# Kernel tuning notes

Measured on AMD Instinct MI355X. Metric: run time of the kernel, lower is better.

## Reference

```python
import jax, jax.numpy as jnp
import numpy as np

B, L, H = 512, 1000, 128


def _lstm_cell(x_t, h, c, w_ih, w_hh, b_ih, b_hh):
    # PyTorch LSTMCell: gates = x @ W_ih^T + b_ih + h @ W_hh^T + b_hh, gate order i,f,g,o
    gates = x_t @ w_ih.T + b_ih + h @ w_hh.T + b_hh  # [B, 4H]
    i, f, g, o = jnp.split(gates, 4, axis=-1)
    i = jax.nn.sigmoid(i)
    f = jax.nn.sigmoid(f)
    g = jnp.tanh(g)
    o = jax.nn.sigmoid(o)
    c_new = f * c + i * g
    h_new = o * jnp.tanh(c_new)
    return h_new, c_new


def setup_inputs() -> dict:
    key = jax.random.key(0)
    ks = jax.random.split(key, 12)
    s = 1.0 / np.sqrt(H)  # torch default uniform(-1/sqrt(H), 1/sqrt(H))
    u = lambda k, shp: jax.random.uniform(k, shp, jnp.float32, -s, s)
    return {
        "x": jax.random.normal(ks[0], (B, L), jnp.float32),
        "w_ih1": u(ks[1], (4 * H, 1)),
        "w_hh1": u(ks[2], (4 * H, H)),
        "b_ih1": u(ks[3], (4 * H,)),
        "b_hh1": u(ks[4], (4 * H,)),
        "w_ih2": u(ks[5], (4 * H, H)),
        "w_hh2": u(ks[6], (4 * H, H)),
        "b_ih2": u(ks[7], (4 * H,)),
        "b_hh2": u(ks[8], (4 * H,)),
        "w_lin": u(ks[9], (1, H)),
        "b_lin": u(ks[10], (1,)),
    }


def reference(x, w_ih1, w_hh1, b_ih1, b_hh1, w_ih2, w_hh2, b_ih2, b_hh2, w_lin, b_lin):
    n = x.shape[0]
    h = w_hh1.shape[1]
    zeros = jnp.zeros((n, h), x.dtype)
    init = (zeros, zeros, zeros, zeros)  # h1, c1, h2, c2

    def step(carry, x_t):
        h1, c1, h2, c2 = carry
        h1, c1 = _lstm_cell(x_t, h1, c1, w_ih1, w_hh1, b_ih1, b_hh1)
        h2, c2 = _lstm_cell(h1, h2, c2, w_ih2, w_hh2, b_ih2, b_hh2)
        out = h2 @ w_lin.T + b_lin  # [B, 1]
        return (h1, c1, h2, c2), out[:, 0]

    xs = x.T[:, :, None]  # [L, B, 1]
    _, outs = jax.lax.scan(step, init, xs)  # outs: [L, B]
    return outs.T  # [B, L]
```

## Files before the change

### kernel.cpp

```cpp
#include <hip/hip_runtime.h>

#define B_ 512
#define L_ 1000
#define H_ 128
#define G_ 512

typedef _Float16 v8h __attribute__((ext_vector_type(8)));
typedef _Float16 h2t __attribute__((ext_vector_type(2)));
typedef float v4f __attribute__((ext_vector_type(4)));

__device__ __forceinline__ float sigmoid_f(float x) {
  return __builtin_amdgcn_rcpf(1.0f + __builtin_amdgcn_exp2f(-1.4426950408889634f * x));
}
__device__ __forceinline__ float tanh_f(float x) {
  return 1.0f - 2.0f * __builtin_amdgcn_rcpf(1.0f + __builtin_amdgcn_exp2f(2.8853900817779268f * x));
}

#define FB_KT 144

#define MFMA16(a, b, c) __builtin_amdgcn_mfma_f32_16x16x32_f16((a), (b), (c), 0, 0, 0)

__global__ __launch_bounds__(512, 2) void lstm_mfma(
    const float* __restrict__ x,
    const float* __restrict__ w_ih1,
    const float* __restrict__ w_hh1,
    const float* __restrict__ b_ih1,
    const float* __restrict__ b_hh1,
    const float* __restrict__ w_ih2,
    const float* __restrict__ w_hh2,
    const float* __restrict__ b_ih2,
    const float* __restrict__ b_hh2,
    const float* __restrict__ w_lin,
    const float* __restrict__ b_lin,
    float* __restrict__ out)
{
  __shared__ __align__(16) float xlds[2][L_];
  __shared__ __align__(16) float olds[2 * L_];
  __shared__ __align__(16) float gbuf1[2][G_];
  __shared__ __align__(16) float gbuf2[2][G_];
  __shared__ __align__(16) unsigned char hb1[4 * FB_KT];
  __shared__ __align__(16) unsigned char hb2[4 * FB_KT];
  __shared__ __align__(16) float wxb[G_];
  __shared__ __align__(16) float bbb1[G_];
  __shared__ __align__(16) float bbb2[G_];
  __shared__ __align__(16) float wlb[H_];

  const int tid  = threadIdx.x;
  const int wv   = tid >> 6;
  const int lane = tid & 63;
  const int quad = lane >> 4;
  const int m15  = lane & 15;
  const int r0   = blockIdx.x * 2;
  const int e    = 2 * lane;

  for (int i = tid; i < 2 * L_; i += 512) ((float*)xlds)[i] = x[r0 * L_ + i];
  ((float*)gbuf1)[tid]       = 0.f;
  ((float*)gbuf1)[tid + 512] = 0.f;
  wxb[tid]  = w_ih1[tid];
  bbb1[tid] = b_ih1[tid] + b_hh1[tid];
  bbb2[tid] = b_ih2[tid] + b_hh2[tid];
  if (tid < H_) wlb[tid] = w_lin[tid];
  if (tid < 144) {
    ((unsigned*)hb1)[tid] = 0u;
    ((unsigned*)hb2)[tid] = 0u;
  }
  const float blv = b_lin[0];

  v8h A1f[4][4], A2if[4][4], A2hf[4][4];
#pragma unroll
  for (int mt = 0; mt < 4; ++mt) {
    const int grow = ((4 * wv + mt) * 16 + m15) * H_;
#pragma unroll
    for (int kt = 0; kt < 4; ++kt) {
      const int koff = kt * 32 + quad * 8;
      float4 a, b;
      a = *(const float4*)(w_hh1 + grow + koff);
      b = *(const float4*)(w_hh1 + grow + koff + 4);
      A1f[mt][kt] = v8h{(_Float16)a.x, (_Float16)a.y, (_Float16)a.z, (_Float16)a.w,
                        (_Float16)b.x, (_Float16)b.y, (_Float16)b.z, (_Float16)b.w};
      a = *(const float4*)(w_ih2 + grow + koff);
      b = *(const float4*)(w_ih2 + grow + koff + 4);
      A2if[mt][kt] = v8h{(_Float16)a.x, (_Float16)a.y, (_Float16)a.z, (_Float16)a.w,
                         (_Float16)b.x, (_Float16)b.y, (_Float16)b.z, (_Float16)b.w};
      a = *(const float4*)(w_hh2 + grow + koff);
      b = *(const float4*)(w_hh2 + grow + koff + 4);
      A2hf[mt][kt] = v8h{(_Float16)a.x, (_Float16)a.y, (_Float16)a.z, (_Float16)a.w,
                         (_Float16)b.x, (_Float16)b.y, (_Float16)b.z, (_Float16)b.w};
    }
  }

  float c1x = 0.f, c1y = 0.f;
  float c2x = 0.f, c2y = 0.f;

  const int hwo = (lane >> 4) * FB_KT + ((lane >> 2) & 3) * 32 + (lane & 3) * 4;
  const int roff = quad * 32 + (m15 & 1) * 16;

  __syncthreads();

  for (int t = 0; t <= L_; ++t) {
    if (tid < 128) {
      if (t < L_) {
        const int row = tid >> 6;
        const float xv = xlds[row][t];
        const float* g1 = gbuf1[row];
        float2 gi = *(const float2*)&g1[e];
        float2 gf = *(const float2*)&g1[128 + e];
        float2 gg = *(const float2*)&g1[256 + e];
        float2 go = *(const float2*)&g1[384 + e];
        float2 wxi = *(const float2*)&wxb[e],       bi = *(const float2*)&bbb1[e];
        float2 wxf = *(const float2*)&wxb[128 + e], bf = *(const float2*)&bbb1[128 + e];
        float2 wxg = *(const float2*)&wxb[256 + e], bg = *(const float2*)&bbb1[256 + e];
        float2 wxo = *(const float2*)&wxb[384 + e], bo = *(const float2*)&bbb1[384 + e];
        float i0 = sigmoid_f(gi.x + wxi.x * xv + bi.x);
        float i1 = sigmoid_f(gi.y + wxi.y * xv + bi.y);
        float f0 = sigmoid_f(gf.x + wxf.x * xv + bf.x);
        float f1 = sigmoid_f(gf.y + wxf.y * xv + bf.y);
        float g0 = tanh_f(gg.x + wxg.x * xv + bg.x);
        float g1v = tanh_f(gg.y + wxg.y * xv + bg.y);
        float o0 = sigmoid_f(go.x + wxo.x * xv + bo.x);
        float o1 = sigmoid_f(go.y + wxo.y * xv + bo.y);
        c1x = f0 * c1x + i0 * g0;
        c1y = f1 * c1y + i1 * g1v;
        h2t hp = h2t{(_Float16)(o0 * tanh_f(c1x)), (_Float16)(o1 * tanh_f(c1y))};
        *(unsigned*)(hb1 + row * 16 + hwo) = __builtin_bit_cast(unsigned, hp);
      }
    } else if (tid < 256) {
      if (t > 0) {
        const int row = (tid >> 6) & 1;
        const float* g2 = gbuf2[row];
        float2 gi = *(const float2*)&g2[e];
        float2 gf = *(const float2*)&g2[128 + e];
        float2 gg = *(const float2*)&g2[256 + e];
        float2 go = *(const float2*)&g2[384 + e];
        float2 bi = *(const float2*)&bbb2[e];
        float2 bf = *(const float2*)&bbb2[128 + e];
        float2 bg = *(const float2*)&bbb2[256 + e];
        float2 bo = *(const float2*)&bbb2[384 + e];
        float i0 = sigmoid_f(gi.x + bi.x);
        float i1 = sigmoid_f(gi.y + bi.y);
        float f0 = sigmoid_f(gf.x + bf.x);
        float f1 = sigmoid_f(gf.y + bf.y);
        float g0 = tanh_f(gg.x + bg.x);
        float g1v = tanh_f(gg.y + bg.y);
        float o0 = sigmoid_f(go.x + bo.x);
        float o1 = sigmoid_f(go.y + bo.y);
        c2x = f0 * c2x + i0 * g0;
        c2y = f1 * c2y + i1 * g1v;
        float h0 = o0 * tanh_f(c2x);
        float h1 = o1 * tanh_f(c2y);
        h2t hp = h2t{(_Float16)h0, (_Float16)h1};
        *(unsigned*)(hb2 + row * 16 + hwo) = __builtin_bit_cast(unsigned, hp);
        float2 wlv = *(const float2*)&wlb[e];
        float p2 = h0 * wlv.x + h1 * wlv.y;
#pragma unroll
        for (int s = 1; s < 64; s <<= 1) p2 += __shfl_xor(p2, s, 64);
        if (lane == 0) olds[row * L_ + (t - 1)] = p2 + blv;
      }
    }
    __syncthreads();

    if (t < L_) {
      v4f a2[4], a1[4];
#pragma unroll
      for (int m = 0; m < 4; ++m) { a2[m] = v4f{0, 0, 0, 0}; a1[m] = v4f{0, 0, 0, 0}; }
      __builtin_amdgcn_s_setprio(1);
#pragma unroll
      for (int kt = 0; kt < 4; ++kt) {
        v8h b1 = *(const v8h*)(hb1 + kt * FB_KT + roff);
        v8h b2 = *(const v8h*)(hb2 + kt * FB_KT + roff);
#pragma unroll
        for (int m = 0; m < 4; ++m) {
          a2[m] = MFMA16(A2if[m][kt], b1, a2[m]);
          a2[m] = MFMA16(A2hf[m][kt], b2, a2[m]);
          a1[m] = MFMA16(A1f[m][kt],  b1, a1[m]);
        }
      }
      __builtin_amdgcn_s_setprio(0);
      if (m15 < 2) {
#pragma unroll
        for (int m = 0; m < 4; ++m) {
          *(v4f*)&gbuf2[m15][(4 * wv + m) * 16 + quad * 4] = a2[m];
          *(v4f*)&gbuf1[m15][(4 * wv + m) * 16 + quad * 4] = a1[m];
        }
      }
    }
    __syncthreads();
  }

  for (int i = tid; i < 2 * L_; i += 512) out[r0 * L_ + i] = olds[i];
}

extern "C" void kernel_launch(void* const* d_in, const int* in_sizes, int n_in,
                              void* d_out, int out_size, void* d_ws, size_t ws_size,
                              hipStream_t stream) {
  const float* x     = (const float*)d_in[0];
  const float* w_ih1 = (const float*)d_in[1];
  const float* w_hh1 = (const float*)d_in[2];
  const float* b_ih1 = (const float*)d_in[3];
  const float* b_hh1 = (const float*)d_in[4];
  const float* w_ih2 = (const float*)d_in[5];
  const float* w_hh2 = (const float*)d_in[6];
  const float* b_ih2 = (const float*)d_in[7];
  const float* b_hh2 = (const float*)d_in[8];
  const float* w_lin = (const float*)d_in[9];
  const float* b_lin = (const float*)d_in[10];

  lstm_mfma<<<B_ / 2, 512, 0, stream>>>(
      x, w_ih1, w_hh1, b_ih1, b_hh1, w_ih2, w_hh2, b_ih2, b_hh2,
      w_lin, b_lin, (float*)d_out);
}
```

Measured before the change: 1.604 ms.

## Overlap LSTM layer elementwise phases with the other layer's MFMA

Splits each timestep's single MFMA phase into two halves. The layer-1 elementwise update now runs alongside the layer-2 gate MFMAs, and the layer-2 elementwise update runs alongside the layer-1 recurrent MFMAs. The h1 fp16 buffer is double-buffered so the layer-2 MFMA can read the previous step's h1 while layer 1 writes the new one. The goal is to stop MFMA-idle waves from waiting behind the serial activation math between barriers. The cost is more complex buffer indexing, and the layer-2 MFMA does one wasted pass at t=0.

Result: slower. 1.733 ms (+8.0%).

```diff
diff --git a/kernel.cpp b/kernel.cpp
--- a/kernel.cpp
+++ b/kernel.cpp
@@ -38,7 +38,7 @@
   __shared__ __align__(16) float olds[2 * L_];
   __shared__ __align__(16) float gbuf1[2][G_];
   __shared__ __align__(16) float gbuf2[2][G_];
-  __shared__ __align__(16) unsigned char hb1[4 * FB_KT];
+  __shared__ __align__(16) unsigned char hb1[2][4 * FB_KT];
   __shared__ __align__(16) unsigned char hb2[4 * FB_KT];
   __shared__ __align__(16) float wxb[G_];
   __shared__ __align__(16) float bbb1[G_];
@@ -60,10 +60,8 @@
   bbb1[tid] = b_ih1[tid] + b_hh1[tid];
   bbb2[tid] = b_ih2[tid] + b_hh2[tid];
   if (tid < H_) wlb[tid] = w_lin[tid];
-  if (tid < 144) {
-    ((unsigned*)hb1)[tid] = 0u;
-    ((unsigned*)hb2)[tid] = 0u;
-  }
+  if (tid < 288) ((unsigned*)hb1)[tid] = 0u;
+  if (tid < 144) ((unsigned*)hb2)[tid] = 0u;
   const float blv = b_lin[0];
 
   v8h A1f[4][4], A2if[4][4], A2hf[4][4];
@@ -98,90 +96,104 @@
   __syncthreads();
 
   for (int t = 0; t <= L_; ++t) {
-    if (tid < 128) {
-      if (t < L_) {
-        const int row = tid >> 6;
-        const float xv = xlds[row][t];
-        const float* g1 = gbuf1[row];
-        float2 gi = *(const float2*)&g1[e];
-        float2 gf = *(const float2*)&g1[128 + e];
-        float2 gg = *(const float2*)&g1[256 + e];
-        float2 go = *(const float2*)&g1[384 + e];
-        float2 wxi = *(const float2*)&wxb[e],       bi = *(const float2*)&bbb1[e];
-        float2 wxf = *(const float2*)&wxb[128 + e], bf = *(const float2*)&bbb1[128 + e];
-        float2 wxg = *(const float2*)&wxb[256 + e], bg = *(const float2*)&bbb1[256 + e];
-        float2 wxo = *(const float2*)&wxb[384 + e], bo = *(const float2*)&bbb1[384 + e];
-        float i0 = sigmoid_f(gi.x + wxi.x * xv + bi.x);
-        float i1 = sigmoid_f(gi.y + wxi.y * xv + bi.y);
-        float f0 = sigmoid_f(gf.x + wxf.x * xv + bf.x);
-        float f1 = sigmoid_f(gf.y + wxf.y * xv + bf.y);
-        float g0 = tanh_f(gg.x + wxg.x * xv + bg.x);
-        float g1v = tanh_f(gg.y + wxg.y * xv + bg.y);
-        float o0 = sigmoid_f(go.x + wxo.x * xv + bo.x);
-        float o1 = sigmoid_f(go.y + wxo.y * xv + bo.y);
-        c1x = f0 * c1x + i0 * g0;
-        c1y = f1 * c1y + i1 * g1v;
-        h2t hp = h2t{(_Float16)(o0 * tanh_f(c1x)), (_Float16)(o1 * tanh_f(c1y))};
-        *(unsigned*)(hb1 + row * 16 + hwo) = __builtin_bit_cast(unsigned, hp);
-      }
-    } else if (tid < 256) {
-      if (t > 0) {
-        const int row = (tid >> 6) & 1;
-        const float* g2 = gbuf2[row];
-        float2 gi = *(const float2*)&g2[e];
-        float2 gf = *(const float2*)&g2[128 + e];
-        float2 gg = *(const float2*)&g2[256 + e];
-        float2 go = *(const float2*)&g2[384 + e];
-        float2 bi = *(const float2*)&bbb2[e];
-        float2 bf = *(const float2*)&bbb2[128 + e];
-        float2 bg = *(const float2*)&bbb2[256 + e];
-        float2 bo = *(const float2*)&bbb2[384 + e];
-        float i0 = sigmoid_f(gi.x + bi.x);
-        float i1 = sigmoid_f(gi.y + bi.y);
-        float f0 = sigmoid_f(gf.x + bf.x);
-        float f1 = sigmoid_f(gf.y + bf.y);
-        float g0 = tanh_f(gg.x + bg.x);
-        float g1v = tanh_f(gg.y + bg.y);
-        float o0 = sigmoid_f(go.x + bo.x);
-        float o1 = sigmoid_f(go.y + bo.y);
-        c2x = f0 * c2x + i0 * g0;
-        c2y = f1 * c2y + i1 * g1v;
-        float h0 = o0 * tanh_f(c2x);
-        float h1 = o1 * tanh_f(c2y);
-        h2t hp = h2t{(_Float16)h0, (_Float16)h1};
-        *(unsigned*)(hb2 + row * 16 + hwo) = __builtin_bit_cast(unsigned, hp);
-        float2 wlv = *(const float2*)&wlb[e];
-        float p2 = h0 * wlv.x + h1 * wlv.y;
-#pragma unroll
-        for (int s = 1; s < 64; s <<= 1) p2 += __shfl_xor(p2, s, 64);
-        if (lane == 0) olds[row * L_ + (t - 1)] = p2 + blv;
-      }
-    }
-    __syncthreads();
-
-    if (t < L_) {
-      v4f a2[4], a1[4];
-#pragma unroll
-      for (int m = 0; m < 4; ++m) { a2[m] = v4f{0, 0, 0, 0}; a1[m] = v4f{0, 0, 0, 0}; }
+    if (tid < 128 && t < L_) {
+      const int row = tid >> 6;
+      const float xv = xlds[row][t];
+      const float* g1 = gbuf1[row];
+      float2 gi = *(const float2*)&g1[e];
+      float2 gf = *(const float2*)&g1[128 + e];
+      float2 gg = *(const float2*)&g1[256 + e];
+      float2 go = *(const float2*)&g1[384 + e];
+      float2 wxi = *(const float2*)&wxb[e],       bi = *(const float2*)&bbb1[e];
+      float2 wxf = *(const float2*)&wxb[128 + e], bf = *(const float2*)&bbb1[128 + e];
+      float2 wxg = *(const float2*)&wxb[256 + e], bg = *(const float2*)&bbb1[256 + e];
+      float2 wxo = *(const float2*)&wxb[384 + e], bo = *(const float2*)&bbb1[384 + e];
+      float i0 = sigmoid_f(gi.x + wxi.x * xv + bi.x);
+      float i1 = sigmoid_f(gi.y + wxi.y * xv + bi.y);
+      float f0 = sigmoid_f(gf.x + wxf.x * xv + bf.x);
+      float f1 = sigmoid_f(gf.y + wxf.y * xv + bf.y);
+      float g0 = tanh_f(gg.x + wxg.x * xv + bg.x);
+      float g1v = tanh_f(gg.y + wxg.y * xv + bg.y);
+      float o0 = sigmoid_f(go.x + wxo.x * xv + bo.x);
+      float o1 = sigmoid_f(go.y + wxo.y * xv + bo.y);
+      c1x = f0 * c1x + i0 * g0;
+      c1y = f1 * c1y + i1 * g1v;
+      h2t hp = h2t{(_Float16)(o0 * tanh_f(c1x)), (_Float16)(o1 * tanh_f(c1y))};
+      *(unsigned*)(&hb1[t & 1][0] + row * 16 + hwo) = __builtin_bit_cast(unsigned, hp);
+    }
+    {
+      v4f a2[4];
+#pragma unroll
+      for (int m = 0; m < 4; ++m) a2[m] = v4f{0, 0, 0, 0};
+      const unsigned char* b1p = &hb1[(t + 1) & 1][0];
       __builtin_amdgcn_s_setprio(1);
 #pragma unroll
       for (int kt = 0; kt < 4; ++kt) {
-        v8h b1 = *(const v8h*)(hb1 + kt * FB_KT + roff);
         v8h b2 = *(const v8h*)(hb2 + kt * FB_KT + roff);
+        v8h b1 = *(const v8h*)(b1p + kt * FB_KT + roff);
 #pragma unroll
         for (int m = 0; m < 4; ++m) {
+          a2[m] = MFMA16(A2hf[m][kt], b2, a2[m]);
           a2[m] = MFMA16(A2if[m][kt], b1, a2[m]);
-          a2[m] = MFMA16(A2hf[m][kt], b2, a2[m]);
-          a1[m] = MFMA16(A1f[m][kt],  b1, a1[m]);
         }
       }
       __builtin_amdgcn_s_setprio(0);
       if (m15 < 2) {
 #pragma unroll
-        for (int m = 0; m < 4; ++m) {
+        for (int m = 0; m < 4; ++m)
           *(v4f*)&gbuf2[m15][(4 * wv + m) * 16 + quad * 4] = a2[m];
+      }
+    }
+    __syncthreads();
+
+    if (tid >= 128 && tid < 256 && t > 0) {
+      const int row = (tid >> 6) & 1;
+      const float* g2 = gbuf2[row];
+      float2 gi = *(const float2*)&g2[e];
+      float2 gf = *(const float2*)&g2[128 + e];
+      float2 gg = *(const float2*)&g2[256 + e];
+      float2 go = *(const float2*)&g2[384 + e];
+      float2 bi = *(const float2*)&bbb2[e];
+      float2 bf = *(const float2*)&bbb2[128 + e];
+      float2 bg = *(const float2*)&bbb2[256 + e];
+      float2 bo = *(const float2*)&bbb2[384 + e];
+      float i0 = sigmoid_f(gi.x + bi.x);
+      float i1 = sigmoid_f(gi.y + bi.y);
+      float f0 = sigmoid_f(gf.x + bf.x);
+      float f1 = sigmoid_f(gf.y + bf.y);
+      float g0 = tanh_f(gg.x + bg.x);
+      float g1v = tanh_f(gg.y + bg.y);
+      float o0 = sigmoid_f(go.x + bo.x);
+      float o1 = sigmoid_f(go.y + bo.y);
+      c2x = f0 * c2x + i0 * g0;
+      c2y = f1 * c2y + i1 * g1v;
+      float h0 = o0 * tanh_f(c2x);
+      float h1 = o1 * tanh_f(c2y);
+      h2t hp = h2t{(_Float16)h0, (_Float16)h1};
+      *(unsigned*)(hb2 + row * 16 + hwo) = __builtin_bit_cast(unsigned, hp);
+      float2 wlv = *(const float2*)&wlb[e];
+      float p2 = h0 * wlv.x + h1 * wlv.y;
+#pragma unroll
+      for (int s = 1; s < 64; s <<= 1) p2 += __shfl_xor(p2, s, 64);
+      if (lane == 0) olds[row * L_ + (t - 1)] = p2 + blv;
+    }
+    if (t < L_) {
+      v4f a1[4];
+#pragma unroll
+      for (int m = 0; m < 4; ++m) a1[m] = v4f{0, 0, 0, 0};
+      const unsigned char* b1p = &hb1[t & 1][0];
+      __builtin_amdgcn_s_setprio(1);
+#pragma unroll
+      for (int kt = 0; kt < 4; ++kt) {
+        v8h b1 = *(const v8h*)(b1p + kt * FB_KT + roff);
+#pragma unroll
+        for (int m = 0; m < 4; ++m) a1[m] = MFMA16(A1f[m][kt], b1, a1[m]);
+      }
+      __builtin_amdgcn_s_setprio(0);
+      if (m15 < 2) {
+#pragma unroll
+        for (int m = 0; m < 4; ++m)
           *(v4f*)&gbuf1[m15][(4 * wv + m) * 16 + quad * 4] = a1[m];
-        }
       }
     }
     __syncthreads();
```

## Fuse LSTM gate activations into MFMA accumulators with gate-interleaved row mapping

Applied to the files above, without the earlier changes.

Weight rows are remapped so each wave's four MFMA tiles hold the i, f, g, o gates for the same 16 hidden units. Each lane can then apply the cell update directly from its accumulator registers, which removes the gbuf round trip through LDS and the separate activation threads. Biases are folded in as the accumulator's initial value, and h buffers are double-buffered in LDS. Layer 1 and layer 2 now run sequentially within a timestep, with two barriers per step. The output projection is reduced with atomicAdd into LDS, which adds LDS atomics and serialises layer 2 behind layer 1 instead of pipelining them across timesteps.

Measured after the change: 2.034 ms. 1.27x slower.

```diff
diff --git a/kernel.cpp b/kernel.cpp
--- a/kernel.cpp
+++ b/kernel.cpp
@@ -6,7 +6,7 @@
 #define G_ 512
 
 typedef _Float16 v8h __attribute__((ext_vector_type(8)));
-typedef _Float16 h2t __attribute__((ext_vector_type(2)));
+typedef _Float16 h4t __attribute__((ext_vector_type(4)));
 typedef float v4f __attribute__((ext_vector_type(4)));
 
 __device__ __forceinline__ float sigmoid_f(float x) {
@@ -36,10 +36,8 @@
 {
   __shared__ __align__(16) float xlds[2][L_];
   __shared__ __align__(16) float olds[2 * L_];
-  __shared__ __align__(16) float gbuf1[2][G_];
-  __shared__ __align__(16) float gbuf2[2][G_];
-  __shared__ __align__(16) unsigned char hb1[4 * FB_KT];
-  __shared__ __align__(16) unsigned char hb2[4 * FB_KT];
+  __shared__ __align__(16) unsigned char hb1[2][4 * FB_KT];
+  __shared__ __align__(16) unsigned char hb2[2][4 * FB_KT];
   __shared__ __align__(16) float wxb[G_];
   __shared__ __align__(16) float bbb1[G_];
   __shared__ __align__(16) float bbb2[G_];
@@ -51,16 +49,16 @@
   const int quad = lane >> 4;
   const int m15  = lane & 15;
   const int r0   = blockIdx.x * 2;
-  const int e    = 2 * lane;
-
-  for (int i = tid; i < 2 * L_; i += 512) ((float*)xlds)[i] = x[r0 * L_ + i];
-  ((float*)gbuf1)[tid]       = 0.f;
-  ((float*)gbuf1)[tid + 512] = 0.f;
+
+  for (int i = tid; i < 2 * L_; i += 512) {
+    ((float*)xlds)[i] = x[r0 * L_ + i];
+    olds[i] = 0.f;
+  }
   wxb[tid]  = w_ih1[tid];
   bbb1[tid] = b_ih1[tid] + b_hh1[tid];
   bbb2[tid] = b_ih2[tid] + b_hh2[tid];
   if (tid < H_) wlb[tid] = w_lin[tid];
-  if (tid < 144) {
+  if (tid < 288) {
     ((unsigned*)hb1)[tid] = 0u;
     ((unsigned*)hb2)[tid] = 0u;
   }
@@ -68,126 +66,128 @@
 
   v8h A1f[4][4], A2if[4][4], A2hf[4][4];
 #pragma unroll
-  for (int mt = 0; mt < 4; ++mt) {
-    const int grow = ((4 * wv + mt) * 16 + m15) * H_;
+  for (int m = 0; m < 4; ++m) {
+    const int grow = ((wv + 8 * m) * 16 + m15) * H_;
 #pragma unroll
     for (int kt = 0; kt < 4; ++kt) {
       const int koff = kt * 32 + quad * 8;
       float4 a, b;
       a = *(const float4*)(w_hh1 + grow + koff);
       b = *(const float4*)(w_hh1 + grow + koff + 4);
-      A1f[mt][kt] = v8h{(_Float16)a.x, (_Float16)a.y, (_Float16)a.z, (_Float16)a.w,
-                        (_Float16)b.x, (_Float16)b.y, (_Float16)b.z, (_Float16)b.w};
+      A1f[m][kt] = v8h{(_Float16)a.x, (_Float16)a.y, (_Float16)a.z, (_Float16)a.w,
+                       (_Float16)b.x, (_Float16)b.y, (_Float16)b.z, (_Float16)b.w};
       a = *(const float4*)(w_ih2 + grow + koff);
       b = *(const float4*)(w_ih2 + grow + koff + 4);
-      A2if[mt][kt] = v8h{(_Float16)a.x, (_Float16)a.y, (_Float16)a.z, (_Float16)a.w,
-                         (_Float16)b.x, (_Float16)b.y, (_Float16)b.z, (_Float16)b.w};
+      A2if[m][kt] = v8h{(_Float16)a.x, (_Float16)a.y, (_Float16)a.z, (_Float16)a.w,
+                        (_Float16)b.x, (_Float16)b.y, (_Float16)b.z, (_Float16)b.w};
       a = *(const float4*)(w_hh2 + grow + koff);
       b = *(const float4*)(w_hh2 + grow + koff + 4);
-      A2hf[mt][kt] = v8h{(_Float16)a.x, (_Float16)a.y, (_Float16)a.z, (_Float16)a.w,
-                         (_Float16)b.x, (_Float16)b.y, (_Float16)b.z, (_Float16)b.w};
-    }
-  }
-
-  float c1x = 0.f, c1y = 0.f;
-  float c2x = 0.f, c2y = 0.f;
-
-  const int hwo = (lane >> 4) * FB_KT + ((lane >> 2) & 3) * 32 + (lane & 3) * 4;
-  const int roff = quad * 32 + (m15 & 1) * 16;
+      A2hf[m][kt] = v8h{(_Float16)a.x, (_Float16)a.y, (_Float16)a.z, (_Float16)a.w,
+                        (_Float16)b.x, (_Float16)b.y, (_Float16)b.z, (_Float16)b.w};
+    }
+  }
+
+  float c10 = 0.f, c11 = 0.f, c12 = 0.f, c13 = 0.f;
+  float c20 = 0.f, c21 = 0.f, c22 = 0.f, c23 = 0.f;
+
+  const int cbase = 16 * wv + 4 * quad;
+  const int roff  = quad * 32 + (m15 & 1) * 16;
+  const int hwo2 = (wv >> 1) * FB_KT + ((16 * (wv & 1) + 4 * quad) >> 3) * 32
+                 + (m15 & 1) * 16 + (quad & 1) * 8;
 
   __syncthreads();
 
-  for (int t = 0; t <= L_; ++t) {
-    if (tid < 128) {
-      if (t < L_) {
-        const int row = tid >> 6;
-        const float xv = xlds[row][t];
-        const float* g1 = gbuf1[row];
-        float2 gi = *(const float2*)&g1[e];
-        float2 gf = *(const float2*)&g1[128 + e];
-        float2 gg = *(const float2*)&g1[256 + e];
-        float2 go = *(const float2*)&g1[384 + e];
-        float2 wxi = *(const float2*)&wxb[e],       bi = *(const float2*)&bbb1[e];
-        float2 wxf = *(const float2*)&wxb[128 + e], bf = *(const float2*)&bbb1[128 + e];
-        float2 wxg = *(const float2*)&wxb[256 + e], bg = *(const float2*)&bbb1[256 + e];
-        float2 wxo = *(const float2*)&wxb[384 + e], bo = *(const float2*)&bbb1[384 + e];
-        float i0 = sigmoid_f(gi.x + wxi.x * xv + bi.x);
-        float i1 = sigmoid_f(gi.y + wxi.y * xv + bi.y);
-        float f0 = sigmoid_f(gf.x + wxf.x * xv + bf.x);
-        float f1 = sigmoid_f(gf.y + wxf.y * xv + bf.y);
-        float g0 = tanh_f(gg.x + wxg.x * xv + bg.x);
-        float g1v = tanh_f(gg.y + wxg.y * xv + bg.y);
-        float o0 = sigmoid_f(go.x + wxo.x * xv + bo.x);
-        float o1 = sigmoid_f(go.y + wxo.y * xv + bo.y);
-        c1x = f0 * c1x + i0 * g0;
-        c1y = f1 * c1y + i1 * g1v;
-        h2t hp = h2t{(_Float16)(o0 * tanh_f(c1x)), (_Float16)(o1 * tanh_f(c1y))};
-        *(unsigned*)(hb1 + row * 16 + hwo) = __builtin_bit_cast(unsigned, hp);
-      }
-    } else if (tid < 256) {
-      if (t > 0) {
-        const int row = (tid >> 6) & 1;
-        const float* g2 = gbuf2[row];
-        float2 gi = *(const float2*)&g2[e];
-        float2 gf = *(const float2*)&g2[128 + e];
-        float2 gg = *(const float2*)&g2[256 + e];
-        float2 go = *(const float2*)&g2[384 + e];
-        float2 bi = *(const float2*)&bbb2[e];
-        float2 bf = *(const float2*)&bbb2[128 + e];
-        float2 bg = *(const float2*)&bbb2[256 + e];
-        float2 bo = *(const float2*)&bbb2[384 + e];
-        float i0 = sigmoid_f(gi.x + bi.x);
-        float i1 = sigmoid_f(gi.y + bi.y);
-        float f0 = sigmoid_f(gf.x + bf.x);
-        float f1 = sigmoid_f(gf.y + bf.y);
-        float g0 = tanh_f(gg.x + bg.x);
-        float g1v = tanh_f(gg.y + bg.y);
-        float o0 = sigmoid_f(go.x + bo.x);
-        float o1 = sigmoid_f(go.y + bo.y);
-        c2x = f0 * c2x + i0 * g0;
-        c2y = f1 * c2y + i1 * g1v;
-        float h0 = o0 * tanh_f(c2x);
-        float h1 = o1 * tanh_f(c2y);
-        h2t hp = h2t{(_Float16)h0, (_Float16)h1};
-        *(unsigned*)(hb2 + row * 16 + hwo) = __builtin_bit_cast(unsigned, hp);
-        float2 wlv = *(const float2*)&wlb[e];
-        float p2 = h0 * wlv.x + h1 * wlv.y;
-#pragma unroll
-        for (int s = 1; s < 64; s <<= 1) p2 += __shfl_xor(p2, s, 64);
-        if (lane == 0) olds[row * L_ + (t - 1)] = p2 + blv;
-      }
-    }
-    __syncthreads();
-
-    if (t < L_) {
-      v4f a2[4], a1[4];
-#pragma unroll
-      for (int m = 0; m < 4; ++m) { a2[m] = v4f{0, 0, 0, 0}; a1[m] = v4f{0, 0, 0, 0}; }
+  for (int t = 0; t < L_; ++t) {
+    v4f a0 = *(const v4f*)&bbb1[cbase];
+    v4f a1 = *(const v4f*)&bbb1[128 + cbase];
+    v4f a2 = *(const v4f*)&bbb1[256 + cbase];
+    v4f a3 = *(const v4f*)&bbb1[384 + cbase];
+    {
+      const unsigned char* bp = &hb1[(t + 1) & 1][0];
       __builtin_amdgcn_s_setprio(1);
 #pragma unroll
       for (int kt = 0; kt < 4; ++kt) {
-        v8h b1 = *(const v8h*)(hb1 + kt * FB_KT + roff);
-        v8h b2 = *(const v8h*)(hb2 + kt * FB_KT + roff);
-#pragma unroll
-        for (int m = 0; m < 4; ++m) {
-          a2[m] = MFMA16(A2if[m][kt], b1, a2[m]);
-          a2[m] = MFMA16(A2hf[m][kt], b2, a2[m]);
-          a1[m] = MFMA16(A1f[m][kt],  b1, a1[m]);
-        }
+        v8h b = *(const v8h*)(bp + kt * FB_KT + roff);
+        a0 = MFMA16(A1f[0][kt], b, a0);
+        a1 = MFMA16(A1f[1][kt], b, a1);
+        a2 = MFMA16(A1f[2][kt], b, a2);
+        a3 = MFMA16(A1f[3][kt], b, a3);
       }
       __builtin_amdgcn_s_setprio(0);
-      if (m15 < 2) {
-#pragma unroll
-        for (int m = 0; m < 4; ++m) {
-          *(v4f*)&gbuf2[m15][(4 * wv + m) * 16 + quad * 4] = a2[m];
-          *(v4f*)&gbuf1[m15][(4 * wv + m) * 16 + quad * 4] = a1[m];
-        }
+    }
+    {
+      const float xv = xlds[m15 & 1][t];
+      v4f wxi = *(const v4f*)&wxb[cbase];
+      v4f wxf = *(const v4f*)&wxb[128 + cbase];
+      v4f wxg = *(const v4f*)&wxb[256 + cbase];
+      v4f wxo = *(const v4f*)&wxb[384 + cbase];
+      float h0, h1, h2, h3;
+      { float iv = sigmoid_f(a0[0] + wxi[0] * xv), fv = sigmoid_f(a1[0] + wxf[0] * xv);
+        float gv = tanh_f(a2[0] + wxg[0] * xv),    ov = sigmoid_f(a3[0] + wxo[0] * xv);
+        c10 = fv * c10 + iv * gv; h0 = ov * tanh_f(c10); }
+      { float iv = sigmoid_f(a0[1] + wxi[1] * xv), fv = sigmoid_f(a1[1] + wxf[1] * xv);
+        float gv = tanh_f(a2[1] + wxg[1] * xv),    ov = sigmoid_f(a3[1] + wxo[1] * xv);
+        c11 = fv * c11 + iv * gv; h1 = ov * tanh_f(c11); }
+      { float iv = sigmoid_f(a0[2] + wxi[2] * xv), fv = sigmoid_f(a1[2] + wxf[2] * xv);
+        float gv = tanh_f(a2[2] + wxg[2] * xv),    ov = sigmoid_f(a3[2] + wxo[2] * xv);
+        c12 = fv * c12 + iv * gv; h2 = ov * tanh_f(c12); }
+      { float iv = sigmoid_f(a0[3] + wxi[3] * xv), fv = sigmoid_f(a1[3] + wxf[3] * xv);
+        float gv = tanh_f(a2[3] + wxg[3] * xv),    ov = sigmoid_f(a3[3] + wxo[3] * xv);
+        c13 = fv * c13 + iv * gv; h3 = ov * tanh_f(c13); }
+      h4t hp = h4t{(_Float16)h0, (_Float16)h1, (_Float16)h2, (_Float16)h3};
+      if (m15 < 2) *(h4t*)(&hb1[t & 1][0] + hwo2) = hp;
+    }
+    __syncthreads();
+
+    v4f d0 = *(const v4f*)&bbb2[cbase];
+    v4f d1 = *(const v4f*)&bbb2[128 + cbase];
+    v4f d2 = *(const v4f*)&bbb2[256 + cbase];
+    v4f d3 = *(const v4f*)&bbb2[384 + cbase];
+    {
+      const unsigned char* p1 = &hb1[t & 1][0];
+      const unsigned char* p2 = &hb2[(t + 1) & 1][0];
+      __builtin_amdgcn_s_setprio(1);
+#pragma unroll
+      for (int kt = 0; kt < 4; ++kt) {
+        v8h b1 = *(const v8h*)(p1 + kt * FB_KT + roff);
+        v8h b2 = *(const v8h*)(p2 + kt * FB_KT + roff);
+        d0 = MFMA16(A2if[0][kt], b1, d0);
+        d1 = MFMA16(A2if[1][kt], b1, d1);
+        d2 = MFMA16(A2if[2][kt], b1, d2);
+        d3 = MFMA16(A2if[3][kt], b1, d3);
+        d0 = MFMA16(A2hf[0][kt], b2, d0);
+        d1 = MFMA16(A2hf[1][kt], b2, d1);
+        d2 = MFMA16(A2hf[2][kt], b2, d2);
+        d3 = MFMA16(A2hf[3][kt], b2, d3);
       }
+      __builtin_amdgcn_s_setprio(0);
+    }
+    {
+      float h0, h1, h2, h3;
+      { float iv = sigmoid_f(d0[0]), fv = sigmoid_f(d1[0]);
+        float gv = tanh_f(d2[0]),    ov = sigmoid_f(d3[0]);
+        c20 = fv * c20 + iv * gv; h0 = ov * tanh_f(c20); }
+      { float iv = sigmoid_f(d0[1]), fv = sigmoid_f(d1[1]);
+        float gv = tanh_f(d2[1]),    ov = sigmoid_f(d3[1]);
+        c21 = fv * c21 + iv * gv; h1 = ov * tanh_f(c21); }
+      { float iv = sigmoid_f(d0[2]), fv = sigmoid_f(d1[2]);
+        float gv = tanh_f(d2[2]),    ov = sigmoid_f(d3[2]);
+        c22 = fv * c22 + iv * gv; h2 = ov * tanh_f(c22); }
+      { float iv = sigmoid_f(d0[3]), fv = sigmoid_f(d1[3]);
+        float gv = tanh_f(d2[3]),    ov = sigmoid_f(d3[3]);
+        c23 = fv * c23 + iv * gv; h3 = ov * tanh_f(c23); }
+      h4t hp = h4t{(_Float16)h0, (_Float16)h1, (_Float16)h2, (_Float16)h3};
+      if (m15 < 2) *(h4t*)(&hb2[t & 1][0] + hwo2) = hp;
+      v4f wlv = *(const v4f*)&wlb[cbase];
+      float p = h0 * wlv[0] + h1 * wlv[1] + h2 * wlv[2] + h3 * wlv[3];
+      p += __shfl_xor(p, 16, 64);
+      p += __shfl_xor(p, 32, 64);
+      if (lane < 2) atomicAdd(&olds[lane * L_ + t], p);
     }
     __syncthreads();
   }
 
-  for (int i = tid; i < 2 * L_; i += 512) out[r0 * L_ + i] = olds[i];
+  for (int i = tid; i < 2 * L_; i += 512) out[r0 * L_ + i] = olds[i] + blv;
 }
 
 extern "C" void kernel_launch(void* const* d_in, const int* in_sizes, int n_in,
```
